# Kernel optimization log

Hardware: AMD Instinct MI355X
Metric: run time of the kernel (lower is better)

Reference implementation:

```python
import jax, jax.numpy as jnp
import numpy as np

EPS = 1e-9  # Dice BatchNorm epsilon

def _dice(x, alpha, mm, mv):
    # Keras BN(center=False, scale=False) in inference mode: (x - moving_mean) / sqrt(moving_var + eps)
    p = jax.nn.sigmoid((x - mm) * jax.lax.rsqrt(mv + EPS))
    return x * (p + alpha * (1.0 - p))

def setup_inputs() -> dict:
    key = jax.random.key(0)
    ks = jax.random.split(key, 8)
    B, T, E = 4096, 200, 12
    return {
        "query": jax.random.normal(ks[0], (B, 1, E), jnp.float32),
        "keys": jax.random.normal(ks[1], (B, T, E), jnp.float32),
        "mask": jnp.ones((B, T), dtype=bool),
        "W0": jax.random.normal(ks[2], (48, 80), jnp.float32) * (1.0 / np.sqrt(48)),
        "b0": jnp.zeros((80,), jnp.float32),
        "W1": jax.random.normal(ks[3], (80, 40), jnp.float32) * (1.0 / np.sqrt(80)),
        "b1": jnp.zeros((40,), jnp.float32),
        "alpha0": jax.random.uniform(ks[4], (80,), jnp.float32),
        "alpha1": jax.random.uniform(ks[5], (40,), jnp.float32),
        "mm0": jnp.zeros((80,), jnp.float32),
        "mv0": jnp.ones((80,), jnp.float32),
        "mm1": jnp.zeros((40,), jnp.float32),
        "mv1": jnp.ones((40,), jnp.float32),
        "atten_kernel": jax.random.normal(ks[6], (40, 1), jnp.float32) * (1.0 / np.sqrt(40)),
        "atten_bias": jnp.zeros((1,), jnp.float32),
    }

def reference(query, keys, mask, W0, b0, W1, b1, alpha0, alpha1,
              mm0, mv0, mm1, mv1, atten_kernel, atten_bias):
    B, T, E = keys.shape
    q = jnp.broadcast_to(query, (B, T, E))  # K.repeat_elements(query, T, 1)
    att = jnp.concatenate([q, keys, q - keys, q * keys], axis=-1)  # [B, T, 4E=48]
    h = _dice(jnp.einsum('bti,io->bto', att, W0) + b0, alpha0, mm0, mv0)  # [B,T,80]
    h = _dice(jnp.einsum('bti,io->bto', h, W1) + b1, alpha1, mm1, mv1)    # [B,T,40]
    score = jnp.einsum('bti,io->bto', h, atten_kernel) + atten_bias       # [B,T,1]
    scores = jnp.swapaxes(score, 1, 2)  # [B,1,T]
    # NOTE: original code computes tf.where(mask,...) but overwrites it and
    # matmuls the UNMASKED scores with keys (bug reproduced faithfully).
    return jnp.matmul(scores, keys)  # [B,1,E]
```

## Files before the change

kernel.cpp:

```cpp
#include <hip/hip_runtime.h>
#include <hip/hip_bf16.h>
#include <math.h>

#define B_TOT 4096
#define T_LEN 200
#define E_DIM 12
#define LOG2E 1.44269504088896340736f

typedef __attribute__((ext_vector_type(8))) short bf16x8;
typedef __attribute__((ext_vector_type(4))) float f32x4;
typedef unsigned short ushort_t;


__device__ inline unsigned short f2bf(float f) {
    union { float f; unsigned u; } x; x.f = f;
    unsigned r = x.u + 0x7FFFu + ((x.u >> 16) & 1u);
    return (unsigned short)(r >> 16);
}
__device__ inline unsigned pk_bf16(float a, float b) {
    float2 t; t.x = a; t.y = b;
    __hip_bfloat162 h = __float22bfloat162_rn(t);
    union { __hip_bfloat162 h; unsigned u; } cv; cv.h = h;
    return cv.u;
}

__global__ __launch_bounds__(256) void din_prep(
    const float* __restrict__ W0, const float* __restrict__ b0v,
    const float* __restrict__ W1, const float* __restrict__ b1v,
    const float* __restrict__ a0, const float* __restrict__ a1,
    const float* __restrict__ mm0, const float* __restrict__ mv0,
    const float* __restrict__ mm1, const float* __restrict__ mv1,
    const float* __restrict__ ak, void* __restrict__ wsv)
{
    unsigned char* wsb = (unsigned char*)wsv;
    ushort_t* w0e2 = (ushort_t*)wsb;
    ushort_t* wq   = (ushort_t*)(wsb + 5120);
    ushort_t* w1e  = (ushort_t*)(wsb + 10240);
    float* d0c = (float*)(wsb + 19456);
    float* d1c = (float*)(wsb + 20736);

    int idx = blockIdx.x * 256 + threadIdx.x;
    if (idx < 2560) {
        int n = idx >> 5, k = idx & 31;
        float v = 0.0f;
        if (k < 12)       v = W0[(12 + k) * 80 + n] - W0[(24 + k) * 80 + n];
        else if (k < 24)  v = W0[(36 + (k - 12)) * 80 + n];
        w0e2[n * 32 + k] = f2bf(v);
    } else if (idx < 5120) {
        int v2 = idx - 2560;
        int n = v2 >> 5, k = v2 & 31;
        float v = 0.0f;
        if (k < 12)       v = W0[k * 80 + n] + W0[(24 + k) * 80 + n];
        else if (k == 12) v = b0v[n];
        wq[n * 32 + k] = f2bf(v);
    } else if (idx < 9728) {
        int v2 = idx - 5120;
        int n = v2 / 96, k = v2 - n * 96;
        float v = 0.0f;
        if (n < 40) {
            if (k < 80)       v = W1[k * 40 + n];
            else if (k == 80) v = b1v[n];
        }
        w1e[n * 96 + k] = f2bf(v);
    } else if (idx < 10048) {
        int v2 = idx - 9728;
        int o = v2 >> 2, c = v2 & 3;
        float rs = rsqrtf(mv0[o] + 1e-9f) * LOG2E;
        float val = (c == 0) ? -rs : (c == 1) ? mm0[o] * rs : (c == 2) ? a0[o] : 1.0f - a0[o];
        d0c[o * 4 + c] = val;
    } else {
        int v2 = idx - 10048;
        int j = v2 >> 2, c = v2 & 3;
        float val = 0.0f;
        if (j < 40) {
            float rs = rsqrtf(mv1[j] + 1e-9f) * LOG2E;
            val = (c == 0) ? -rs : (c == 1) ? mm1[j] * rs : (c == 2) ? a1[j] * ak[j]
                                                          : (1.0f - a1[j]) * ak[j];
        }
        d1c[j * 4 + c] = val;
    }
}

#define A0_STR 40
#define H_STR  104

__global__ __launch_bounds__(256, 2) void din_mfma(
    const float* __restrict__ query, const float* __restrict__ keys,
    const float* __restrict__ abias_p, const void* __restrict__ wsv,
    float* __restrict__ out)
{
    __shared__ __align__(16) ushort_t Aseg[4 * 64];
    __shared__ __align__(16) ushort_t A0[4 * 64 * A0_STR];
    __shared__ __align__(16) ushort_t H[4 * 16 * H_STR];
    const unsigned char* wsb = (const unsigned char*)wsv;
    const ushort_t* w0e2 = (const ushort_t*)wsb;
    const ushort_t* wq   = (const ushort_t*)(wsb + 5120);
    const ushort_t* w1e  = (const ushort_t*)(wsb + 10240);
    const f32x4* d0cp = (const f32x4*)(wsb + 19456);
    const f32x4* d1cp = (const f32x4*)(wsb + 20736);

    const int tid = threadIdx.x;
    const int lane = tid & 63;
    const int w = tid >> 6;
    const int l15 = lane & 15;
    const int quad = lane >> 4;
    const int b = blockIdx.x * 4 + w;

    ushort_t* A0w = &A0[w * 64 * A0_STR];
    ushort_t* Hw  = &H[w * 16 * H_STR];
    ushort_t* Asw = &Aseg[w * 64];

    bf16x8 b0f[5];
    #pragma unroll
    for (int nt = 0; nt < 5; ++nt)
        b0f[nt] = *(const bf16x8*)(w0e2 + (nt * 16 + l15) * 32 + quad * 8);
    bf16x8 b1f[3][3];
    #pragma unroll
    for (int nt = 0; nt < 3; ++nt)
        #pragma unroll
        for (int ks = 0; ks < 3; ++ks)
            b1f[nt][ks] = *(const bf16x8*)(w1e + (nt * 16 + l15) * 96 + ks * 32 + quad * 8);
    f32x4 d0c[5];
    #pragma unroll
    for (int nt = 0; nt < 5; ++nt) d0c[nt] = d0cp[nt * 16 + l15];
    f32x4 d1c[3];
    #pragma unroll
    for (int nt = 0; nt < 3; ++nt) d1c[nt] = d1cp[nt * 16 + l15];

    float qq[12];
    {
        const float4* qp = (const float4*)(query + (size_t)b * E_DIM);
        float4 q0 = qp[0], q1 = qp[1], q2 = qp[2];
        qq[0]=q0.x; qq[1]=q0.y; qq[2]=q0.z; qq[3]=q0.w;
        qq[4]=q1.x; qq[5]=q1.y; qq[6]=q1.z; qq[7]=q1.w;
        qq[8]=q0.x*0.f+q2.x; qq[9]=q2.y; qq[10]=q2.z; qq[11]=q2.w;
    }

    float z0q[5];
    {
        unsigned p01 = pk_bf16(qq[0], qq[1]), p23 = pk_bf16(qq[2], qq[3]);
        unsigned p45 = pk_bf16(qq[4], qq[5]), p67 = pk_bf16(qq[6], qq[7]);
        unsigned p89 = pk_bf16(qq[8], qq[9]), pab = pk_bf16(qq[10], qq[11]);
        union { unsigned u[4]; bf16x8 v; } qa;
        qa.u[0] = (quad == 0) ? p01 : (quad == 1) ? p89 : 0u;
        qa.u[1] = (quad == 0) ? p23 : (quad == 1) ? pab : 0u;
        qa.u[2] = (quad == 0) ? p45 : (quad == 1) ? 0x00003F80u : 0u;
        qa.u[3] = (quad == 0) ? p67 : 0u;
        #pragma unroll
        for (int nt = 0; nt < 5; ++nt) {
            bf16x8 wf = *(const bf16x8*)(wq + (nt * 16 + l15) * 32 + quad * 8);
            f32x4 zz = {0.f, 0.f, 0.f, 0.f};
            zz = __builtin_amdgcn_mfma_f32_16x16x32_bf16(qa.v, wf, zz, 0, 0, 0);
            z0q[nt] = zz[0];
        }
    }
    const float abias = abias_p[0];

    if (quad == 0) {
        bf16x8 one8 = {(short)0x3F80, 0, 0, 0, 0, 0, 0, 0};
        bf16x8 zero8 = {0, 0, 0, 0, 0, 0, 0, 0};
        *(bf16x8*)(Hw + l15 * H_STR + 80) = one8;
        *(bf16x8*)(Hw + l15 * H_STR + 88) = zero8;
    }

    f32x4 acc2 = {0.f, 0.f, 0.f, 0.f};

    for (int c = 0; c < 4; ++c) {
        const int t0 = c * 64;
        const int myT = t0 + lane;
        const bool valid = myT < T_LEN;

        float kk[12];
        if (valid) {
            const float4* kp = (const float4*)(keys + ((size_t)b * T_LEN + myT) * E_DIM);
            float4 k0 = kp[0], k1 = kp[1], k2 = kp[2];
            kk[0]=k0.x; kk[1]=k0.y; kk[2]=k0.z; kk[3]=k0.w;
            kk[4]=k1.x; kk[5]=k1.y; kk[6]=k1.z; kk[7]=k1.w;
            kk[8]=k2.x; kk[9]=k2.y; kk[10]=k2.z; kk[11]=k2.w;
        } else {
            #pragma unroll
            for (int i = 0; i < 12; ++i) kk[i] = 0.0f;
        }
        {
            unsigned kw[6], qkw[6];
            #pragma unroll
            for (int i = 0; i < 6; ++i)
                kw[i] = pk_bf16(kk[2 * i], kk[2 * i + 1]);
            #pragma unroll
            for (int i = 0; i < 6; ++i)
                qkw[i] = pk_bf16(qq[2 * i] * kk[2 * i], qq[2 * i + 1] * kk[2 * i + 1]);
            uint4* dst = (uint4*)(A0w + lane * A0_STR);
            uint4 v0, v1, v2, v3;
            v0.x = kw[0];  v0.y = kw[1];  v0.z = kw[2];  v0.w = kw[3];
            v1.x = kw[4];  v1.y = kw[5];  v1.z = qkw[0]; v1.w = qkw[1];
            v2.x = qkw[2]; v2.y = qkw[3]; v2.z = qkw[4]; v2.w = qkw[5];
            v3.x = 0u;     v3.y = 0u;     v3.z = 0u;     v3.w = 0u;
            dst[0] = v0; dst[1] = v1; dst[2] = v2; dst[3] = v3;
        }
        Asw[lane] = 0;

        const int ntiles = (c < 3) ? 4 : 1;
        for (int ti = 0; ti < ntiles; ++ti) {
            bf16x8 a0 = *(const bf16x8*)(A0w + (ti * 16 + l15) * A0_STR + quad * 8);
            f32x4 acc[5];
            #pragma unroll
            for (int nt = 0; nt < 5; ++nt) {
                f32x4 cc = {0.f, 0.f, 0.f, 0.f};
                acc[nt] = __builtin_amdgcn_mfma_f32_16x16x32_bf16(a0, b0f[nt], cc, 0, 0, 0);
            }
            #pragma unroll
            for (int nt = 0; nt < 5; ++nt) {
                #pragma unroll
                for (int r = 0; r < 4; ++r) {
                    float z = acc[nt][r] + z0q[nt];
                    float pg = __builtin_amdgcn_rcpf(
                        1.0f + __builtin_amdgcn_exp2f(fmaf(z, d0c[nt].x, d0c[nt].y)));
                    float h = z * fmaf(pg, d0c[nt].w, d0c[nt].z);
                    Hw[(quad * 4 + r) * H_STR + nt * 16 + l15] = f2bf(h);
                }
            }
            bf16x8 af[3];
            #pragma unroll
            for (int ks = 0; ks < 3; ++ks)
                af[ks] = *(const bf16x8*)(Hw + l15 * H_STR + ks * 32 + quad * 8);
            float s[4] = {0.f, 0.f, 0.f, 0.f};
            #pragma unroll
            for (int nt = 0; nt < 3; ++nt) {
                f32x4 cc = {0.f, 0.f, 0.f, 0.f};
                #pragma unroll
                for (int ks = 0; ks < 3; ++ks)
                    cc = __builtin_amdgcn_mfma_f32_16x16x32_bf16(af[ks], b1f[nt][ks], cc, 0, 0, 0);
                #pragma unroll
                for (int r = 0; r < 4; ++r) {
                    float z = cc[r];
                    float pg = __builtin_amdgcn_rcpf(
                        1.0f + __builtin_amdgcn_exp2f(fmaf(z, d1c[nt].x, d1c[nt].y)));
                    s[r] = fmaf(z, fmaf(pg, d1c[nt].w, d1c[nt].z), s[r]);
                }
            }
            #pragma unroll
            for (int m = 1; m < 16; m <<= 1) {
                #pragma unroll
                for (int r = 0; r < 4; ++r) s[r] += __shfl_xor(s[r], m, 64);
            }
            if (l15 == 0) {
                unsigned long long pk = 0ull;
                #pragma unroll
                for (int r = 0; r < 4; ++r) {
                    int t = t0 + ti * 16 + quad * 4 + r;
                    unsigned short sb = (t < T_LEN) ? f2bf(s[r] + abias) : (unsigned short)0;
                    pk |= (unsigned long long)sb << (16 * r);
                }
                *(unsigned long long*)(Asw + ti * 16 + quad * 4) = pk;
            }
        }

        #pragma unroll
        for (int ks = 0; ks < 2; ++ks) {
            bf16x8 pa = *(const bf16x8*)(Asw + l15 * 64 + ks * 32 + quad * 8);
            bf16x8 bk;
            #pragma unroll
            for (int j = 0; j < 8; ++j)
                bk[j] = (short)A0w[(ks * 32 + quad * 8 + j) * A0_STR + l15];
            acc2 = __builtin_amdgcn_mfma_f32_16x16x32_bf16(pa, bk, acc2, 0, 0, 0);
        }
    }

    if (quad == 0 && l15 < 12)
        out[(size_t)b * E_DIM + l15] = acc2[0];
}

extern "C" void kernel_launch(void* const* d_in, const int* in_sizes, int n_in,
                              void* d_out, int out_size, void* d_ws, size_t ws_size,
                              hipStream_t stream) {
    const float* query = (const float*)d_in[0];
    const float* keys  = (const float*)d_in[1];
    const float* W0  = (const float*)d_in[3];
    const float* b0v = (const float*)d_in[4];
    const float* W1  = (const float*)d_in[5];
    const float* b1v = (const float*)d_in[6];
    const float* a0  = (const float*)d_in[7];
    const float* a1  = (const float*)d_in[8];
    const float* mm0 = (const float*)d_in[9];
    const float* mv0 = (const float*)d_in[10];
    const float* mm1 = (const float*)d_in[11];
    const float* mv1 = (const float*)d_in[12];
    const float* ak  = (const float*)d_in[13];
    const float* ab  = (const float*)d_in[14];
    float* out = (float*)d_out;

    hipLaunchKernelGGL(din_prep, dim3(40), dim3(256), 0, stream,
                       W0, b0v, W1, b1v, a0, a1, mm0, mv0, mm1, mv1, ak, d_ws);
    hipLaunchKernelGGL(din_mfma, dim3(B_TOT / 4), dim3(256), 0, stream,
                       query, keys, ab, d_ws, out);
}
```

Baseline: 149.0 us.

## Raise occupancy: move Dice constants to LDS, fold bias into MFMA accumulator

Raises the launch-bounds occupancy hint from 2 to 4 blocks per CU and moves the per-column Dice constants from registers into shared memory, loaded once per block behind a new barrier, to cut register pressure. The query-side layer-0 bias is folded into the MFMA accumulator init, so the per-tile acc[5] array is no longer kept live. bf16 conversion now uses packed hardware converts in place of manual rounding. This adds per-tile LDS reads and one __syncthreads, and the tighter register budget may cause spills.

```diff
diff --git a/kernel.cpp b/kernel.cpp
--- a/kernel.cpp
+++ b/kernel.cpp
@@ -84,7 +84,7 @@
 #define A0_STR 40
 #define H_STR  104
 
-__global__ __launch_bounds__(256, 2) void din_mfma(
+__global__ __launch_bounds__(256, 4) void din_mfma(
     const float* __restrict__ query, const float* __restrict__ keys,
     const float* __restrict__ abias_p, const void* __restrict__ wsv,
     float* __restrict__ out)
@@ -92,6 +92,8 @@
     __shared__ __align__(16) ushort_t Aseg[4 * 64];
     __shared__ __align__(16) ushort_t A0[4 * 64 * A0_STR];
     __shared__ __align__(16) ushort_t H[4 * 16 * H_STR];
+    __shared__ __align__(16) f32x4 d0cL[80];
+    __shared__ __align__(16) f32x4 d1cL[48];
     const unsigned char* wsb = (const unsigned char*)wsv;
     const ushort_t* w0e2 = (const ushort_t*)wsb;
     const ushort_t* wq   = (const ushort_t*)(wsb + 5120);
@@ -109,6 +111,9 @@
     ushort_t* A0w = &A0[w * 64 * A0_STR];
     ushort_t* Hw  = &H[w * 16 * H_STR];
     ushort_t* Asw = &Aseg[w * 64];
+
+    if (tid < 80)        d0cL[tid] = d0cp[tid];
+    else if (tid < 128)  d1cL[tid - 80] = d1cp[tid - 80];
 
     bf16x8 b0f[5];
     #pragma unroll
@@ -120,12 +125,6 @@
         #pragma unroll
         for (int ks = 0; ks < 3; ++ks)
             b1f[nt][ks] = *(const bf16x8*)(w1e + (nt * 16 + l15) * 96 + ks * 32 + quad * 8);
-    f32x4 d0c[5];
-    #pragma unroll
-    for (int nt = 0; nt < 5; ++nt) d0c[nt] = d0cp[nt * 16 + l15];
-    f32x4 d1c[3];
-    #pragma unroll
-    for (int nt = 0; nt < 3; ++nt) d1c[nt] = d1cp[nt * 16 + l15];
 
     float qq[12];
     {
@@ -133,7 +132,7 @@
         float4 q0 = qp[0], q1 = qp[1], q2 = qp[2];
         qq[0]=q0.x; qq[1]=q0.y; qq[2]=q0.z; qq[3]=q0.w;
         qq[4]=q1.x; qq[5]=q1.y; qq[6]=q1.z; qq[7]=q1.w;
-        qq[8]=q0.x*0.f+q2.x; qq[9]=q2.y; qq[10]=q2.z; qq[11]=q2.w;
+        qq[8]=q2.x; qq[9]=q2.y; qq[10]=q2.z; qq[11]=q2.w;
     }
 
     float z0q[5];
@@ -163,6 +162,8 @@
         *(bf16x8*)(Hw + l15 * H_STR + 88) = zero8;
     }
 
+    __syncthreads();
+
     f32x4 acc2 = {0.f, 0.f, 0.f, 0.f};
 
     for (int c = 0; c < 4; ++c) {
@@ -202,23 +203,30 @@
         const int ntiles = (c < 3) ? 4 : 1;
         for (int ti = 0; ti < ntiles; ++ti) {
             bf16x8 a0 = *(const bf16x8*)(A0w + (ti * 16 + l15) * A0_STR + quad * 8);
-            f32x4 acc[5];
+
             #pragma unroll
             for (int nt = 0; nt < 5; ++nt) {
-                f32x4 cc = {0.f, 0.f, 0.f, 0.f};
-                acc[nt] = __builtin_amdgcn_mfma_f32_16x16x32_bf16(a0, b0f[nt], cc, 0, 0, 0);
-            }
-            #pragma unroll
-            for (int nt = 0; nt < 5; ++nt) {
+                float zq = z0q[nt];
+                f32x4 cc = {zq, zq, zq, zq};
+                cc = __builtin_amdgcn_mfma_f32_16x16x32_bf16(a0, b0f[nt], cc, 0, 0, 0);
+                f32x4 dc = d0cL[nt * 16 + l15];
+                float h[4];
                 #pragma unroll
                 for (int r = 0; r < 4; ++r) {
-                    float z = acc[nt][r] + z0q[nt];
+                    float z = cc[r];
                     float pg = __builtin_amdgcn_rcpf(
-                        1.0f + __builtin_amdgcn_exp2f(fmaf(z, d0c[nt].x, d0c[nt].y)));
-                    float h = z * fmaf(pg, d0c[nt].w, d0c[nt].z);
-                    Hw[(quad * 4 + r) * H_STR + nt * 16 + l15] = f2bf(h);
+                        1.0f + __builtin_amdgcn_exp2f(fmaf(z, dc.x, dc.y)));
+                    h[r] = z * fmaf(pg, dc.w, dc.z);
                 }
+                unsigned u01 = pk_bf16(h[0], h[1]);
+                unsigned u23 = pk_bf16(h[2], h[3]);
+                ushort_t* hcol = Hw + (quad * 4) * H_STR + nt * 16 + l15;
+                hcol[0 * H_STR] = (ushort_t)u01;
+                hcol[1 * H_STR] = (ushort_t)(u01 >> 16);
+                hcol[2 * H_STR] = (ushort_t)u23;
+                hcol[3 * H_STR] = (ushort_t)(u23 >> 16);
             }
+
             bf16x8 af[3];
             #pragma unroll
             for (int ks = 0; ks < 3; ++ks)
@@ -230,12 +238,13 @@
                 #pragma unroll
                 for (int ks = 0; ks < 3; ++ks)
                     cc = __builtin_amdgcn_mfma_f32_16x16x32_bf16(af[ks], b1f[nt][ks], cc, 0, 0, 0);
+                f32x4 dc1 = d1cL[nt * 16 + l15];
                 #pragma unroll
                 for (int r = 0; r < 4; ++r) {
                     float z = cc[r];
                     float pg = __builtin_amdgcn_rcpf(
-                        1.0f + __builtin_amdgcn_exp2f(fmaf(z, d1c[nt].x, d1c[nt].y)));
-                    s[r] = fmaf(z, fmaf(pg, d1c[nt].w, d1c[nt].z), s[r]);
+                        1.0f + __builtin_amdgcn_exp2f(fmaf(z, dc1.x, dc1.y)));
+                    s[r] = fmaf(z, fmaf(pg, dc1.w, dc1.z), s[r]);
                 }
             }
             #pragma unroll
@@ -244,13 +253,14 @@
                 for (int r = 0; r < 4; ++r) s[r] += __shfl_xor(s[r], m, 64);
             }
             if (l15 == 0) {
-                unsigned long long pk = 0ull;
-                #pragma unroll
-                for (int r = 0; r < 4; ++r) {
-                    int t = t0 + ti * 16 + quad * 4 + r;
-                    unsigned short sb = (t < T_LEN) ? f2bf(s[r] + abias) : (unsigned short)0;
-                    pk |= (unsigned long long)sb << (16 * r);
-                }
+                const int tb = t0 + ti * 16 + quad * 4;
+                float v0 = (tb + 0 < T_LEN) ? s[0] + abias : 0.0f;
+                float v1 = (tb + 1 < T_LEN) ? s[1] + abias : 0.0f;
+                float v2 = (tb + 2 < T_LEN) ? s[2] + abias : 0.0f;
+                float v3 = (tb + 3 < T_LEN) ? s[3] + abias : 0.0f;
+                unsigned lo = pk_bf16(v0, v1), hi = pk_bf16(v2, v3);
+                unsigned long long pk = (unsigned long long)lo
+                                      | ((unsigned long long)hi << 32);
                 *(unsigned long long*)(Asw + ti * 16 + quad * 4) = pk;
             }
         }
```

After: 184.6 us. 23.9% more time.
